# Performance work log

Measured on AMD Instinct MI355X. Metric: run time of the kernel, lower is better.

The kernel has to match this reference:

```python
import jax, jax.numpy as jnp
import numpy as np

INPUT_DIM = 66
OUTPUT_COUNT = 8192
NUM_PAIRS = 65536

def setup_inputs() -> dict:
    key = jax.random.key(0)
    k1, k2, k3, k4 = jax.random.split(key, 4)
    x = jax.random.normal(k1, (NUM_PAIRS, INPUT_DIM), dtype=jnp.float32)
    query = jax.random.normal(k2, (OUTPUT_COUNT, INPUT_DIM), dtype=jnp.float32)
    # nn.Linear(input_dim, input_dim): weight [out,in], bias [out]
    bound = 1.0 / np.sqrt(INPUT_DIM)
    Wk = jax.random.uniform(k3, (INPUT_DIM, INPUT_DIM), minval=-bound, maxval=bound, dtype=jnp.float32)
    bk = jax.random.uniform(k4, (INPUT_DIM,), minval=-bound, maxval=bound, dtype=jnp.float32)
    return {"x": x, "query": query, "Wk": Wk, "bk": bk}

def reference(x, query, Wk, bk):
    # K = Linear(x): x @ Wk^T + bk  -> [num_pairs, d]
    K = x @ Wk.T + bk
    # scores: [output_count, num_pairs]
    scores = jnp.einsum("qd,nd->qn", query, K)
    attn = jax.nn.softmax(scores, axis=1)
    # selected: [output_count, d] — note values are raw x, not K
    selected = attn @ x
    return selected
```

## Files before the change

### kernel.cpp

```cpp
#include <hip/hip_runtime.h>
#include <cstdint>


typedef __bf16    bf16x4 __attribute__((ext_vector_type(4)));
typedef __bf16    bf16x8 __attribute__((ext_vector_type(8)));
typedef _Float16  f16x4  __attribute__((ext_vector_type(4)));
typedef _Float16  f16x8  __attribute__((ext_vector_type(8)));
typedef float     f32x2  __attribute__((ext_vector_type(2)));
typedef float     f32x16 __attribute__((ext_vector_type(16)));

extern "C" __device__ float __ocml_native_exp2_f32(float);

#define NUM_PAIRS   65536
#define NUM_Q       8192
#define DIM         66
#define QPITCH      80
#define KFT         2560
#define XFT         3072
#define PARTP       68
#define NS          16
#define NTILES      (NUM_PAIRS/32)

__device__ __forceinline__ f32x16 mfma_bf16(bf16x8 a, bf16x8 b, f32x16 c) {
    return __builtin_amdgcn_mfma_f32_32x32x16_bf16(a, b, c, 0, 0, 0);
}
__device__ __forceinline__ f32x16 mfma_f16(f16x8 a, f16x8 b, f32x16 c) {
    return __builtin_amdgcn_mfma_f32_32x32x16_f16(a, b, c, 0, 0, 0);
}
__device__ __forceinline__ void plswap(unsigned &a, unsigned &b) {
    asm volatile("s_nop 1\n\t"
                 "v_permlane32_swap_b32 %0, %1\n\t"
                 "s_nop 1"
                 : "+v"(a), "+v"(b));
}
__device__ __forceinline__ unsigned packbf(float a, float b) {
    union { __bf16 h[2]; unsigned u; } t;
    t.h[0] = (__bf16)a; t.h[1] = (__bf16)b;
    return t.u;
}
union U4 { unsigned u[4]; bf16x8 v; };

__device__ __forceinline__ void makefrags(const f32x16 &s, U4 *f) {
    float P[16];
    #pragma unroll
    for (int r = 0; r < 16; ++r) P[r] = __ocml_native_exp2_f32(s[r]);
    unsigned E0 = packbf(P[0],  P[1]),  E1 = packbf(P[2],  P[3]);
    unsigned F0 = packbf(P[4],  P[5]),  F1 = packbf(P[6],  P[7]);
    plswap(E0, F0); plswap(E1, F1);
    f[0].u[0] = E0; f[0].u[1] = E1; f[0].u[2] = F0; f[0].u[3] = F1;
    unsigned G0 = packbf(P[8],  P[9]),  G1 = packbf(P[10], P[11]);
    unsigned H0 = packbf(P[12], P[13]), H1 = packbf(P[14], P[15]);
    plswap(G0, H0); plswap(G1, H1);
    f[1].u[0] = G0; f[1].u[1] = G1; f[1].u[2] = H0; f[1].u[3] = H1;
}

__device__ __forceinline__ void pipe_step(
    int t, int tiles, const _Float16* __restrict__ kf, const __bf16* __restrict__ xf,
    f16x8 (&kPre)[5], const f16x8 (&kNext)[5], bf16x8 (&xR)[6],
    const f16x8 (&aQ)[2][5], f32x16 &s0, f32x16 &s1, f32x16 (&o)[2][3]) {

    {
        long tk = (t + 2 < tiles) ? (long)(t + 2) : (long)(tiles - 1);
        const _Float16* kp = kf + tk * KFT;
        #pragma unroll
        for (int kk = 0; kk < 5; ++kk) kPre[kk] = *(const f16x8*)(kp + kk * 512);
    }
    U4 f0[2];
    makefrags(s0, f0);
    {
        f32x16 ns = {};
        #pragma unroll
        for (int kk = 0; kk < 5; ++kk) ns = mfma_f16(kNext[kk], aQ[0][kk], ns);
        s0 = ns;
    }
    U4 f1[2];
    makefrags(s1, f1);
    {
        f32x16 ns = {};
        #pragma unroll
        for (int kk = 0; kk < 5; ++kk) ns = mfma_f16(kNext[kk], aQ[1][kk], ns);
        s1 = ns;
    }
    #pragma unroll
    for (int par = 0; par < 2; ++par)
        #pragma unroll
        for (int dt = 0; dt < 3; ++dt)
            o[0][dt] = mfma_bf16(f0[par].v, xR[par * 3 + dt], o[0][dt]);
    #pragma unroll
    for (int par = 0; par < 2; ++par)
        #pragma unroll
        for (int dt = 0; dt < 3; ++dt)
            o[1][dt] = mfma_bf16(f1[par].v, xR[par * 3 + dt], o[1][dt]);

    {
        long tx = (t + 1 < tiles) ? (long)(t + 1) : (long)(tiles - 1);
        const __bf16* xp = xf + tx * XFT;
        #pragma unroll
        for (int c = 0; c < 6; ++c) xR[c] = *(const bf16x8*)(xp + c * 512);
    }
}

#define PAP 104
__global__ __launch_bounds__(256) void prep_kernel(
    const float* __restrict__ x, const float* __restrict__ query,
    const float* __restrict__ Wk,
    unsigned short* __restrict__ Af_u, unsigned short* __restrict__ Xf_u,
    unsigned short* __restrict__ Qh_u) {
    const int tid = threadIdx.x;
    const int lane = tid & 63, w = tid >> 6;
    const int l31 = lane & 31, h = lane >> 5;

    if (blockIdx.x >= 512) {
        __shared__ _Float16 sq[128 * PAP];
        __shared__ _Float16 sWT[96 * PAP];
        _Float16* Qh = (_Float16*)Qh_u;
        const long q0 = (long)(blockIdx.x - 512) * 128;

        for (int i = tid; i < 128 * PAP / 2; i += 256) ((unsigned*)sq)[i] = 0u;
        for (int i = tid; i < 96 * PAP / 2; i += 256)  ((unsigned*)sWT)[i] = 0u;
        __syncthreads();

        for (int i = tid; i < 128 * 33; i += 256) {
            int r = i / 33, c2 = (i % 33) * 2;
            f32x2 v = *(const f32x2*)&query[(q0 + r) * DIM + c2];
            sq[r * PAP + c2]     = (_Float16)v.x;
            sq[r * PAP + c2 + 1] = (_Float16)v.y;
        }
        for (int i = tid; i < DIM * 33; i += 256) {
            int d = i / 33, e2 = (i % 33) * 2;
            f32x2 v = *(const f32x2*)&Wk[d * DIM + e2];
            sWT[e2 * PAP + d]       = (_Float16)(v.x * 1.4426950408889634f);
            sWT[(e2 + 1) * PAP + d] = (_Float16)(v.y * 1.4426950408889634f);
        }
        __syncthreads();

        #pragma unroll
        for (int nt = 0; nt < 3; ++nt) {
            f32x16 acc = {};
            #pragma unroll
            for (int kk = 0; kk < 6; ++kk) {
                f16x8 a = *(const f16x8*)&sq[(w * 32 + l31) * PAP + kk * 16 + h * 8];
                f16x8 b = *(const f16x8*)&sWT[(nt * 32 + l31) * PAP + kk * 16 + h * 8];
                acc = mfma_f16(a, b, acc);
            }
            int c = nt * 32 + l31;
            if (c < QPITCH) {
                #pragma unroll
                for (int r = 0; r < 16; ++r) {
                    int row = (r & 3) + 8 * (r >> 2) + 4 * h;
                    Qh[(q0 + w * 32 + row) * QPITCH + c] = (_Float16)acc[r];
                }
            }
        }
        return;
    }

    _Float16* Af = (_Float16*)Af_u;
    __bf16*   Xf = (__bf16*)Xf_u;
    __shared__ _Float16 sxh[128 * PAP];
    const long n0 = (long)blockIdx.x * 128;

    for (int i = tid; i < 128 * PAP / 2; i += 256) ((unsigned*)sxh)[i] = 0u;
    __syncthreads();
    for (int i = tid; i < 128 * 33; i += 256) {
        int r = i / 33, c2 = (i % 33) * 2;
        f32x2 v = *(const f32x2*)&x[(n0 + r) * DIM + c2];
        sxh[r * PAP + c2]     = (_Float16)v.x;
        sxh[r * PAP + c2 + 1] = (_Float16)v.y;
    }
    for (int r = tid; r < 128; r += 256) sxh[r * PAP + DIM] = (_Float16)1.0f;
    __syncthreads();

    for (int i = 0; i < 5; ++i) {
        int slot = i * 256 + tid;
        int tt = slot / 320, rem = slot % 320;
        int kk = rem / 64, l = rem % 64;
        const _Float16* src = &sxh[(32 * tt + (l & 31)) * PAP + kk * 16 + (l >> 5) * 8];
        f16x4 lo = *(const f16x4*)src;
        f16x4 hi = *(const f16x4*)(src + 4);
        f16x8 v = __builtin_shufflevector(lo, hi, 0, 1, 2, 3, 4, 5, 6, 7);
        *(f16x8*)&Af[((long)blockIdx.x * 4 + tt) * KFT + kk * 512 + l * 8] = v;
    }
    for (int i = 0; i < 6; ++i) {
        int slot = i * 256 + tid;
        int tt = slot / 384, rem = slot % 384;
        int c = rem / 64, l = rem % 64;
        int dt = c % 3, par = c / 3;
        int d = 32 * dt + (l & 31);
        int p0 = 32 * tt + 16 * par + 8 * (l >> 5);
        bf16x8 v;
        #pragma unroll
        for (int j = 0; j < 8; ++j)
            v[j] = (__bf16)(float)sxh[(p0 + j) * PAP + d];
        *(bf16x8*)&Xf[((long)blockIdx.x * 4 + tt) * XFT + c * 512 + l * 8] = v;
    }
}

__global__ __launch_bounds__(256, 2) void flash_kernel(
    const unsigned short* __restrict__ Qh_u, const unsigned short* __restrict__ Af_u,
    const unsigned short* __restrict__ Xf_u, unsigned short* __restrict__ Part_u) {
    const _Float16* Qh = (const _Float16*)Qh_u;
    const _Float16* Af = (const _Float16*)Af_u;
    const __bf16*   Xf = (const __bf16*)Xf_u;
    __bf16* Part = (__bf16*)Part_u;

    const int tid = threadIdx.x;
    const int lane = tid & 63, wave = tid >> 6;
    const int l31 = lane & 31, h = lane >> 5;
    const int qb = blockIdx.x / NS, ns = blockIdx.x % NS;
    const int tiles = NTILES / NS;
    const int qbase = qb * 256 + wave * 64;

    const _Float16* kf = Af + (long)(ns * tiles) * KFT + lane * 8;
    const __bf16*   xf = Xf + (long)(ns * tiles) * XFT + lane * 8;

    f16x8 aQ[2][5];
    #pragma unroll
    for (int qt = 0; qt < 2; ++qt)
        #pragma unroll
        for (int kk = 0; kk < 5; ++kk)
            aQ[qt][kk] = *(const f16x8*)&Qh[(long)(qbase + qt * 32 + l31) * QPITCH + kk * 16 + h * 8];

    f32x16 o[2][3] = {};
    f16x8  kA[5], kB[5];
    bf16x8 xR[6];
    f32x16 s0, s1;

    #pragma unroll
    for (int kk = 0; kk < 5; ++kk) kA[kk] = *(const f16x8*)(kf + kk * 512);
    #pragma unroll
    for (int c = 0; c < 6; ++c)    xR[c]  = *(const bf16x8*)(xf + c * 512);
    #pragma unroll
    for (int kk = 0; kk < 5; ++kk) kB[kk] = *(const f16x8*)(kf + KFT + kk * 512);
    {
        f32x16 a = {}, b = {};
        #pragma unroll
        for (int kk = 0; kk < 5; ++kk) {
            a = mfma_f16(kA[kk], aQ[0][kk], a);
            b = mfma_f16(kA[kk], aQ[1][kk], b);
        }
        s0 = a; s1 = b;
    }

    for (int t = 0; t < tiles; t += 2) {
        pipe_step(t,     tiles, kf, xf, kA, kB, xR, aQ, s0, s1, o);
        pipe_step(t + 1, tiles, kf, xf, kB, kA, xR, aQ, s0, s1, o);
    }

    #pragma unroll
    for (int qt = 0; qt < 2; ++qt)
        #pragma unroll
        for (int dt = 0; dt < 3; ++dt)
            #pragma unroll
            for (int r = 0; r < 16; ++r) {
                int row = (r & 3) + 8 * (r >> 2) + 4 * h;
                int q = qbase + qt * 32 + row;
                int d = dt * 32 + l31;
                if (d < DIM + 1)
                    Part[((long)q * NS + ns) * PARTP + d] = (__bf16)o[qt][dt][r];
            }
}

__global__ __launch_bounds__(256) void combine_kernel(
    const unsigned short* __restrict__ Part_u, float* __restrict__ out) {
    const __bf16* Part = (const __bf16*)Part_u;
    int q = blockIdx.x * 2 + (threadIdx.x >> 7);
    int d = threadIdx.x & 127;
    if (d >= DIM) return;
    const __bf16* base = Part + (long)q * NS * PARTP;
    float num = 0.f, den = 0.f;
    #pragma unroll 4
    for (int s = 0; s < NS; ++s) {
        num += (float)base[s * PARTP + d];
        den += (float)base[s * PARTP + DIM];
    }
    out[(long)q * DIM + d] = num / den;
}

extern "C" void kernel_launch(void* const* d_in, const int* in_sizes, int n_in,
                              void* d_out, int out_size, void* d_ws, size_t ws_size,
                              hipStream_t stream) {
    const float* x     = (const float*)d_in[0];
    const float* query = (const float*)d_in[1];
    const float* Wk    = (const float*)d_in[2];
    float* out = (float*)d_out;
    char* ws = (char*)d_ws;

    unsigned short* Qh   = (unsigned short*)(ws + 0);
    unsigned short* Af   = (unsigned short*)(ws + 1310720);
    unsigned short* Xf   = (unsigned short*)(ws + 11796480);
    unsigned short* Part = (unsigned short*)(ws + 24379392);

    prep_kernel<<<512 + NUM_Q / 128, 256, 0, stream>>>(x, query, Wk, Af, Xf, Qh);
    flash_kernel<<<(NUM_Q / 256) * NS, 256, 0, stream>>>(Qh, Af, Xf, Part);
    combine_kernel<<<NUM_Q / 2, 256, 0, stream>>>(Part, out);
}
```

Before: 269.3 us.

## Stage K and X tiles through LDS with double-buffered direct global-to-LDS loads

```diff
diff --git a/kernel.cpp b/kernel.cpp
--- a/kernel.cpp
+++ b/kernel.cpp
@@ -21,6 +21,12 @@
 #define NS          16
 #define NTILES      (NUM_PAIRS/32)
 
+#define KBYTES      5120
+#define XBYTES      6144
+#define CHUNK_K     (2*KBYTES)
+#define CHUNK_X     (2*XBYTES)
+#define CHUNK_BYTES (CHUNK_K+CHUNK_X)
+
 __device__ __forceinline__ f32x16 mfma_bf16(bf16x8 a, bf16x8 b, f32x16 c) {
     return __builtin_amdgcn_mfma_f32_32x32x16_bf16(a, b, c, 0, 0, 0);
 }
@@ -39,6 +45,13 @@
     return t.u;
 }
 union U4 { unsigned u[4]; bf16x8 v; };
+
+__device__ __forceinline__ void gload16(const void* g, void* l) {
+    __builtin_amdgcn_global_load_lds(
+        (const __attribute__((address_space(1))) unsigned int*)g,
+        (__attribute__((address_space(3))) unsigned int*)l,
+        16, 0, 0);
+}
 
 __device__ __forceinline__ void makefrags(const f32x16 &s, U4 *f) {
     float P[16];
@@ -54,52 +67,6 @@
     f[1].u[0] = G0; f[1].u[1] = G1; f[1].u[2] = H0; f[1].u[3] = H1;
 }
 
-__device__ __forceinline__ void pipe_step(
-    int t, int tiles, const _Float16* __restrict__ kf, const __bf16* __restrict__ xf,
-    f16x8 (&kPre)[5], const f16x8 (&kNext)[5], bf16x8 (&xR)[6],
-    const f16x8 (&aQ)[2][5], f32x16 &s0, f32x16 &s1, f32x16 (&o)[2][3]) {
-
-    {
-        long tk = (t + 2 < tiles) ? (long)(t + 2) : (long)(tiles - 1);
-        const _Float16* kp = kf + tk * KFT;
-        #pragma unroll
-        for (int kk = 0; kk < 5; ++kk) kPre[kk] = *(const f16x8*)(kp + kk * 512);
-    }
-    U4 f0[2];
-    makefrags(s0, f0);
-    {
-        f32x16 ns = {};
-        #pragma unroll
-        for (int kk = 0; kk < 5; ++kk) ns = mfma_f16(kNext[kk], aQ[0][kk], ns);
-        s0 = ns;
-    }
-    U4 f1[2];
-    makefrags(s1, f1);
-    {
-        f32x16 ns = {};
-        #pragma unroll
-        for (int kk = 0; kk < 5; ++kk) ns = mfma_f16(kNext[kk], aQ[1][kk], ns);
-        s1 = ns;
-    }
-    #pragma unroll
-    for (int par = 0; par < 2; ++par)
-        #pragma unroll
-        for (int dt = 0; dt < 3; ++dt)
-            o[0][dt] = mfma_bf16(f0[par].v, xR[par * 3 + dt], o[0][dt]);
-    #pragma unroll
-    for (int par = 0; par < 2; ++par)
-        #pragma unroll
-        for (int dt = 0; dt < 3; ++dt)
-            o[1][dt] = mfma_bf16(f1[par].v, xR[par * 3 + dt], o[1][dt]);
-
-    {
-        long tx = (t + 1 < tiles) ? (long)(t + 1) : (long)(tiles - 1);
-        const __bf16* xp = xf + tx * XFT;
-        #pragma unroll
-        for (int c = 0; c < 6; ++c) xR[c] = *(const bf16x8*)(xp + c * 512);
-    }
-}
-
 #define PAP 104
 __global__ __launch_bounds__(256) void prep_kernel(
     const float* __restrict__ x, const float* __restrict__ query,
@@ -211,8 +178,31 @@
     const int tiles = NTILES / NS;
     const int qbase = qb * 256 + wave * 64;
 
-    const _Float16* kf = Af + (long)(ns * tiles) * KFT + lane * 8;
-    const __bf16*   xf = Xf + (long)(ns * tiles) * XFT + lane * 8;
+    const char* Kg = (const char*)(Af + (long)(ns * tiles) * KFT);
+    const char* Xg = (const char*)(Xf + (long)(ns * tiles) * XFT);
+
+    __shared__ __align__(16) char smem[2 * CHUNK_BYTES];
+
+    auto stage = [&](int m, int pb) {
+        char* bK = smem + pb * CHUNK_BYTES;
+        char* bX = bK + CHUNK_K;
+        long ka = (2 * m + 1 < tiles) ? 2 * m + 1 : tiles - 1;
+        long kb = (2 * m + 2 < tiles) ? 2 * m + 2 : tiles - 1;
+        long xa = (2 * m     < tiles) ? 2 * m     : tiles - 1;
+        long xb = (2 * m + 1 < tiles) ? 2 * m + 1 : tiles - 1;
+        gload16(Kg + ka * KBYTES + tid * 16, bK + tid * 16);
+        gload16(Kg + kb * KBYTES + tid * 16, bK + KBYTES + tid * 16);
+        gload16(Xg + xa * XBYTES + tid * 16, bX + tid * 16);
+        gload16(Xg + xb * XBYTES + tid * 16, bX + XBYTES + tid * 16);
+        if (tid < 64) {
+            gload16(Kg + ka * KBYTES + 4096 + tid * 16, bK + 4096 + tid * 16);
+            gload16(Kg + kb * KBYTES + 4096 + tid * 16, bK + KBYTES + 4096 + tid * 16);
+        }
+        if (tid < 128) {
+            gload16(Xg + xa * XBYTES + 4096 + tid * 16, bX + 4096 + tid * 16);
+            gload16(Xg + xb * XBYTES + 4096 + tid * 16, bX + XBYTES + 4096 + tid * 16);
+        }
+    };
 
     f16x8 aQ[2][5];
     #pragma unroll
@@ -222,17 +212,14 @@
             aQ[qt][kk] = *(const f16x8*)&Qh[(long)(qbase + qt * 32 + l31) * QPITCH + kk * 16 + h * 8];
 
     f32x16 o[2][3] = {};
-    f16x8  kA[5], kB[5];
-    bf16x8 xR[6];
     f32x16 s0, s1;
 
-    #pragma unroll
-    for (int kk = 0; kk < 5; ++kk) kA[kk] = *(const f16x8*)(kf + kk * 512);
-    #pragma unroll
-    for (int c = 0; c < 6; ++c)    xR[c]  = *(const bf16x8*)(xf + c * 512);
-    #pragma unroll
-    for (int kk = 0; kk < 5; ++kk) kB[kk] = *(const f16x8*)(kf + KFT + kk * 512);
+    stage(0, 0);
     {
+        f16x8 kA[5];
+        #pragma unroll
+        for (int kk = 0; kk < 5; ++kk)
+            kA[kk] = *(const f16x8*)(Kg + kk * 1024 + lane * 16);
         f32x16 a = {}, b = {};
         #pragma unroll
         for (int kk = 0; kk < 5; ++kk) {
@@ -241,10 +228,52 @@
         }
         s0 = a; s1 = b;
     }
-
-    for (int t = 0; t < tiles; t += 2) {
-        pipe_step(t,     tiles, kf, xf, kA, kB, xR, aQ, s0, s1, o);
-        pipe_step(t + 1, tiles, kf, xf, kB, kA, xR, aQ, s0, s1, o);
+    __syncthreads();
+
+    for (int c = 0; c < tiles / 2; ++c) {
+        if (c + 1 < tiles / 2) stage(c + 1, (c + 1) & 1);
+        const char* bK = smem + (c & 1) * CHUNK_BYTES;
+        const char* bX = bK + CHUNK_K;
+        #pragma unroll
+        for (int p = 0; p < 2; ++p) {
+            f16x8 kR[5];
+            #pragma unroll
+            for (int kk = 0; kk < 5; ++kk)
+                kR[kk] = *(const f16x8*)(bK + p * KBYTES + kk * 1024 + lane * 16);
+            bf16x8 xR[6];
+            #pragma unroll
+            for (int cc = 0; cc < 6; ++cc)
+                xR[cc] = *(const bf16x8*)(bX + p * XBYTES + cc * 1024 + lane * 16);
+
+            U4 f0[2];
+            makefrags(s0, f0);
+            {
+                f32x16 nsv = {};
+                #pragma unroll
+                for (int kk = 0; kk < 5; ++kk) nsv = mfma_f16(kR[kk], aQ[0][kk], nsv);
+                s0 = nsv;
+            }
+            #pragma unroll
+            for (int par = 0; par < 2; ++par)
+                #pragma unroll
+                for (int dt = 0; dt < 3; ++dt)
+                    o[0][dt] = mfma_bf16(f0[par].v, xR[par * 3 + dt], o[0][dt]);
+
+            U4 f1[2];
+            makefrags(s1, f1);
+            {
+                f32x16 nsv = {};
+                #pragma unroll
+                for (int kk = 0; kk < 5; ++kk) nsv = mfma_f16(kR[kk], aQ[1][kk], nsv);
+                s1 = nsv;
+            }
+            #pragma unroll
+            for (int par = 0; par < 2; ++par)
+                #pragma unroll
+                for (int dt = 0; dt < 3; ++dt)
+                    o[1][dt] = mfma_bf16(f1[par].v, xR[par * 3 + dt], o[1][dt]);
+        }
+        __syncthreads();
     }
 
     #pragma unroll
```

After: 249.7 us (median of 2 runs). 7.3% less time.

## Stage X tiles through double-buffered LDS via global_load_lds, share across waves

Applied to the files above, without the earlier changes.

```diff
diff --git a/kernel.cpp b/kernel.cpp
--- a/kernel.cpp
+++ b/kernel.cpp
@@ -21,6 +21,9 @@
 #define NS          16
 #define NTILES      (NUM_PAIRS/32)
 
+#define XBYTES      6144
+#define CHUNK_X     (2*XBYTES)
+
 __device__ __forceinline__ f32x16 mfma_bf16(bf16x8 a, bf16x8 b, f32x16 c) {
     return __builtin_amdgcn_mfma_f32_32x32x16_bf16(a, b, c, 0, 0, 0);
 }
@@ -39,6 +42,13 @@
     return t.u;
 }
 union U4 { unsigned u[4]; bf16x8 v; };
+
+__device__ __forceinline__ void gload16(const void* g, void* l) {
+    __builtin_amdgcn_global_load_lds(
+        (const __attribute__((address_space(1))) unsigned int*)g,
+        (__attribute__((address_space(3))) unsigned int*)l,
+        16, 0, 0);
+}
 
 __device__ __forceinline__ void makefrags(const f32x16 &s, U4 *f) {
     float P[16];
@@ -52,52 +62,6 @@
     unsigned H0 = packbf(P[12], P[13]), H1 = packbf(P[14], P[15]);
     plswap(G0, H0); plswap(G1, H1);
     f[1].u[0] = G0; f[1].u[1] = G1; f[1].u[2] = H0; f[1].u[3] = H1;
-}
-
-__device__ __forceinline__ void pipe_step(
-    int t, int tiles, const _Float16* __restrict__ kf, const __bf16* __restrict__ xf,
-    f16x8 (&kPre)[5], const f16x8 (&kNext)[5], bf16x8 (&xR)[6],
-    const f16x8 (&aQ)[2][5], f32x16 &s0, f32x16 &s1, f32x16 (&o)[2][3]) {
-
-    {
-        long tk = (t + 2 < tiles) ? (long)(t + 2) : (long)(tiles - 1);
-        const _Float16* kp = kf + tk * KFT;
-        #pragma unroll
-        for (int kk = 0; kk < 5; ++kk) kPre[kk] = *(const f16x8*)(kp + kk * 512);
-    }
-    U4 f0[2];
-    makefrags(s0, f0);
-    {
-        f32x16 ns = {};
-        #pragma unroll
-        for (int kk = 0; kk < 5; ++kk) ns = mfma_f16(kNext[kk], aQ[0][kk], ns);
-        s0 = ns;
-    }
-    U4 f1[2];
-    makefrags(s1, f1);
-    {
-        f32x16 ns = {};
-        #pragma unroll
-        for (int kk = 0; kk < 5; ++kk) ns = mfma_f16(kNext[kk], aQ[1][kk], ns);
-        s1 = ns;
-    }
-    #pragma unroll
-    for (int par = 0; par < 2; ++par)
-        #pragma unroll
-        for (int dt = 0; dt < 3; ++dt)
-            o[0][dt] = mfma_bf16(f0[par].v, xR[par * 3 + dt], o[0][dt]);
-    #pragma unroll
-    for (int par = 0; par < 2; ++par)
-        #pragma unroll
-        for (int dt = 0; dt < 3; ++dt)
-            o[1][dt] = mfma_bf16(f1[par].v, xR[par * 3 + dt], o[1][dt]);
-
-    {
-        long tx = (t + 1 < tiles) ? (long)(t + 1) : (long)(tiles - 1);
-        const __bf16* xp = xf + tx * XFT;
-        #pragma unroll
-        for (int c = 0; c < 6; ++c) xR[c] = *(const bf16x8*)(xp + c * 512);
-    }
 }
 
 #define PAP 104
@@ -209,10 +173,21 @@
     const int l31 = lane & 31, h = lane >> 5;
     const int qb = blockIdx.x / NS, ns = blockIdx.x % NS;
     const int tiles = NTILES / NS;
+    const int nchunks = tiles / 2;
     const int qbase = qb * 256 + wave * 64;
 
     const _Float16* kf = Af + (long)(ns * tiles) * KFT + lane * 8;
-    const __bf16*   xf = Xf + (long)(ns * tiles) * XFT + lane * 8;
+    const char*     Xg = (const char*)(Xf + (long)(ns * tiles) * XFT);
+
+    __shared__ __align__(16) char smem[2 * CHUNK_X];
+
+    auto stageX = [&](int m, int pb) {
+        char* b = smem + pb * CHUNK_X;
+        const char* g = Xg + (long)(2 * m) * XBYTES;
+        #pragma unroll
+        for (int r = 0; r < 3; ++r)
+            gload16(g + r * 4096 + tid * 16, b + r * 4096 + tid * 16);
+    };
 
     f16x8 aQ[2][5];
     #pragma unroll
@@ -223,13 +198,11 @@
 
     f32x16 o[2][3] = {};
     f16x8  kA[5], kB[5];
-    bf16x8 xR[6];
     f32x16 s0, s1;
 
+    stageX(0, 0);
     #pragma unroll
     for (int kk = 0; kk < 5; ++kk) kA[kk] = *(const f16x8*)(kf + kk * 512);
-    #pragma unroll
-    for (int c = 0; c < 6; ++c)    xR[c]  = *(const bf16x8*)(xf + c * 512);
     #pragma unroll
     for (int kk = 0; kk < 5; ++kk) kB[kk] = *(const f16x8*)(kf + KFT + kk * 512);
     {
@@ -241,10 +214,56 @@
         }
         s0 = a; s1 = b;
     }
-
-    for (int t = 0; t < tiles; t += 2) {
-        pipe_step(t,     tiles, kf, xf, kA, kB, xR, aQ, s0, s1, o);
-        pipe_step(t + 1, tiles, kf, xf, kB, kA, xR, aQ, s0, s1, o);
+    __syncthreads();
+
+    auto tilestep = [&](int t, const char* xbase, f16x8 (&kPre)[5],
+                        const f16x8 (&kNext)[5]) {
+        {
+            long tk = (t + 2 < tiles) ? (long)(t + 2) : (long)(tiles - 1);
+            const _Float16* kp = kf + tk * KFT;
+            #pragma unroll
+            for (int kk = 0; kk < 5; ++kk) kPre[kk] = *(const f16x8*)(kp + kk * 512);
+        }
+        bf16x8 xR[6];
+        #pragma unroll
+        for (int cc = 0; cc < 6; ++cc)
+            xR[cc] = *(const bf16x8*)(xbase + cc * 1024 + lane * 16);
+
+        U4 f0[2];
+        makefrags(s0, f0);
+        {
+            f32x16 nsv = {};
+            #pragma unroll
+            for (int kk = 0; kk < 5; ++kk) nsv = mfma_f16(kNext[kk], aQ[0][kk], nsv);
+            s0 = nsv;
+        }
+        #pragma unroll
+        for (int par = 0; par < 2; ++par)
+            #pragma unroll
+            for (int dt = 0; dt < 3; ++dt)
+                o[0][dt] = mfma_bf16(f0[par].v, xR[par * 3 + dt], o[0][dt]);
+
+        U4 f1[2];
+        makefrags(s1, f1);
+        {
+            f32x16 nsv = {};
+            #pragma unroll
+            for (int kk = 0; kk < 5; ++kk) nsv = mfma_f16(kNext[kk], aQ[1][kk], nsv);
+            s1 = nsv;
+        }
+        #pragma unroll
+        for (int par = 0; par < 2; ++par)
+            #pragma unroll
+            for (int dt = 0; dt < 3; ++dt)
+                o[1][dt] = mfma_bf16(f1[par].v, xR[par * 3 + dt], o[1][dt]);
+    };
+
+    for (int c = 0; c < nchunks; ++c) {
+        if (c + 1 < nchunks) stageX(c + 1, (c + 1) & 1);
+        const char* bX = smem + (c & 1) * CHUNK_X;
+        tilestep(2 * c,     bX,          kA, kB);
+        tilestep(2 * c + 1, bX + XBYTES, kB, kA);
+        __syncthreads();
     }
 
     #pragma unroll
```

New measurement: 261.3 us. -3.0%, faster.
